# Kernel tuning notes

Measured on AMD Instinct MI355X. Metric: run time of the kernel, lower is better.

The kernel has to match this reference:

```python
import jax, jax.numpy as jnp
import numpy as np

N = 100000
D = 64
E = 1600000
EPS = 1e-5


def setup_inputs() -> dict:
    key = jax.random.key(0)
    k1, k2, k3, k4, k5, k6 = jax.random.split(key, 6)
    node_features = jax.random.normal(k1, (N, D), dtype=jnp.float32)
    edge_index = jax.random.randint(k2, (E, 2), 0, N, dtype=jnp.int64)
    # torch Linear params: W [out, in], b [out]
    lim_m = 1.0 / np.sqrt(2 * D)
    W_msg = jax.random.uniform(k3, (D, 2 * D), minval=-lim_m, maxval=lim_m, dtype=jnp.float32)
    b_msg = jax.random.uniform(k4, (D,), minval=-lim_m, maxval=lim_m, dtype=jnp.float32)
    W_upd = jax.random.uniform(k5, (D, 2 * D), minval=-lim_m, maxval=lim_m, dtype=jnp.float32)
    b_upd = jax.random.uniform(k6, (D,), minval=-lim_m, maxval=lim_m, dtype=jnp.float32)
    gamma = jnp.ones((D,), dtype=jnp.float32)
    beta = jnp.zeros((D,), dtype=jnp.float32)
    return {
        "node_features": node_features,
        "edge_index": edge_index,
        "W_msg": W_msg,
        "b_msg": b_msg,
        "W_upd": W_upd,
        "b_upd": b_upd,
        "gamma": gamma,
        "beta": beta,
    }


def _layer_norm(x, gamma, beta):
    mu = jnp.mean(x, axis=-1, keepdims=True)
    var = jnp.mean(jnp.square(x - mu), axis=-1, keepdims=True)
    return (x - mu) * jax.lax.rsqrt(var + EPS) * gamma + beta


def reference(node_features, edge_index, W_msg, b_msg, W_upd, b_upd, gamma, beta):
    src = edge_index[:, 0]
    tgt = edge_index[:, 1]
    # per-edge message: relu(Linear(cat(x[src], x[tgt])))  -- split weight to avoid [E,2D] concat
    Wm_s = W_msg[:, :D]  # [D, D] applied to src feats
    Wm_t = W_msg[:, D:]  # [D, D] applied to tgt feats
    msg = jax.nn.relu(node_features[src] @ Wm_s.T + node_features[tgt] @ Wm_t.T + b_msg)  # [E, D]
    # scatter-mean into target nodes
    messages = jax.ops.segment_sum(msg, tgt, num_segments=N)  # [N, D]
    counts = jax.ops.segment_sum(jnp.ones((edge_index.shape[0],), dtype=node_features.dtype), tgt, num_segments=N)
    counts = jnp.maximum(counts, 1.0)[:, None]
    messages = messages / counts
    # update: relu(Linear(cat(x, messages))) + residual + LayerNorm
    Wu_x = W_upd[:, :D]
    Wu_m = W_upd[:, D:]
    updated = jax.nn.relu(node_features @ Wu_x.T + messages @ Wu_m.T + b_upd)
    return _layer_norm(updated + node_features, gamma, beta)
```

## Files before the change

### kernel.cpp

```cpp
#include <hip/hip_runtime.h>
#include <hip/hip_bf16.h>
#include <stdint.h>

#define NNODES 100000
#define DF 64
#define NEDGES 1600000
#define ND (NNODES * DF)
#define BKT 100
#define NBUCK 1000
#define CHUNK 128
#define NCHUNK (NEDGES / CHUNK)

static __device__ __forceinline__ float bf2f(unsigned short u) {
    union { uint32_t i; float f; } c; c.i = ((uint32_t)u) << 16; return c.f;
}
static __device__ __forceinline__ void unpack2(uint32_t u, float& lo, float& hi) {
    union { uint32_t i; float f; } a, b;
    a.i = u << 16; b.i = u & 0xFFFF0000u;
    lo = a.f; hi = b.f;
}

__global__ void detect_k(const unsigned short* __restrict__ x,
                         const unsigned int* __restrict__ ei,
                         int* __restrict__ flags) {
    __shared__ int cnt_sane, cnt_odd_nz;
    if (threadIdx.x == 0) { cnt_sane = 0; cnt_odd_nz = 0; }
    __syncthreads();
    unsigned short s = x[threadIdx.x * 2];
    unsigned short m = s & 0x7FFF;
    if (m < 0x0080 || (m >= 0x3000 && m <= 0x4200)) atomicAdd(&cnt_sane, 1);
    if (threadIdx.x < 64) {
        if (ei[threadIdx.x * 2 + 1] != 0u) atomicAdd(&cnt_odd_nz, 1);
    }
    __syncthreads();
    if (threadIdx.x == 0) {
        flags[0] = (cnt_sane >= 192) ? 1 : 0;
        flags[1] = (cnt_odd_nz == 0) ? 1 : 0;
    }
}

__global__ void wconv_k(const int* __restrict__ flags,
                        const void* __restrict__ Wm, const void* __restrict__ Wu,
                        const void* __restrict__ bm, const void* __restrict__ bu,
                        const void* __restrict__ ga, const void* __restrict__ be,
                        float* __restrict__ WfM, float* __restrict__ WfU,
                        float* __restrict__ prm) {
    const int bf = flags[0];
    int i = blockIdx.x * 256 + threadIdx.x;
    if (i < 16384) {
        const void* src = (i < 8192) ? Wm : Wu;
        float* dst = (i < 8192) ? WfM : WfU;
        int ii = i & 8191, j = ii >> 6, k = ii & 63;
        int si = (j & 63) * 128 + ((j >> 6) ? 64 : 0) + k;
        dst[ii] = bf ? bf2f(((const unsigned short*)src)[si]) : ((const float*)src)[si];
    } else if (i < 16384 + 256) {
        int t = i - 16384, which = t >> 6, k = t & 63;
        const void* p = (which == 0) ? bm : (which == 1) ? bu : (which == 2) ? ga : be;
        prm[t] = bf ? bf2f(((const unsigned short*)p)[k]) : ((const float*)p)[k];
    }
}

__global__ __launch_bounds__(256) void proj_k(const int* __restrict__ flags,
                                              const void* __restrict__ xv,
                                              const float* __restrict__ WfM,
                                              const float* __restrict__ prm,
                                              __hip_bfloat16* __restrict__ Ps,
                                              __hip_bfloat16* __restrict__ Pt) {
    const int bf = flags[0];
    const int lane = threadIdx.x & 63;
    const int wib = __builtin_amdgcn_readfirstlane(threadIdx.x >> 6);

    float wsr[64], wtr[64];
    {
        const float* r0 = WfM + lane * 64;
        const float* r1 = WfM + (64 + lane) * 64;
        #pragma unroll
        for (int k = 0; k < 64; ++k) { wsr[k] = r0[k]; wtr[k] = r1[k]; }
    }
    const float bm = prm[lane];

    for (int n = blockIdx.x * 4 + wib; n < NNODES; n += gridDim.x * 4) {
        float as0 = 0.f, as1 = 0.f, at0 = 0.f, at1 = 0.f;
        if (bf) {
            const uint32_t* xw = (const uint32_t*)((const unsigned short*)xv + (size_t)n * DF);
            #pragma unroll
            for (int d = 0; d < 32; ++d) {
                float x0, x1; unpack2(xw[d], x0, x1);
                as0 = fmaf(x0, wsr[2*d],   as0);
                as1 = fmaf(x1, wsr[2*d+1], as1);
                at0 = fmaf(x0, wtr[2*d],   at0);
                at1 = fmaf(x1, wtr[2*d+1], at1);
            }
        } else {
            const float* xf = (const float*)xv + (size_t)n * DF;
            #pragma unroll
            for (int d = 0; d < 64; d += 2) {
                as0 = fmaf(xf[d],   wsr[d],   as0);
                as1 = fmaf(xf[d+1], wsr[d+1], as1);
                at0 = fmaf(xf[d],   wtr[d],   at0);
                at1 = fmaf(xf[d+1], wtr[d+1], at1);
            }
        }
        Ps[(size_t)n * DF + lane] = __float2bfloat16(as0 + as1);
        Pt[(size_t)n * DF + lane] = __float2bfloat16(at0 + at1 + bm);
    }
}

__global__ __launch_bounds__(256) void bhist_k(const int* __restrict__ flags,
                                               const int* __restrict__ ei,
                                               int* __restrict__ BktCnt) {
    __shared__ int h[NBUCK];
    const int i64 = flags[1];
    for (int i = threadIdx.x; i < NBUCK; i += 256) h[i] = 0;
    __syncthreads();
    int stride = gridDim.x * 256;
    for (int e = blockIdx.x * 256 + threadIdx.x; e < NEDGES; e += stride) {
        int tgt = i64 ? ei[4*e + 2] : ei[2*e + 1];
        if ((unsigned)tgt < NNODES) atomicAdd(&h[tgt / BKT], 1);
    }
    __syncthreads();
    for (int b = threadIdx.x; b < NBUCK; b += 256)
        if (h[b]) atomicAdd(BktCnt + b, h[b]);
}

__global__ __launch_bounds__(1024) void bscan_k(const int* __restrict__ BktCnt,
                                                int* __restrict__ BktOff,
                                                int* __restrict__ BktCur) {
    __shared__ int lds[1024];
    int t = threadIdx.x;
    int c = (t < NBUCK) ? BktCnt[t] : 0;
    lds[t] = c;
    __syncthreads();
    for (int off = 1; off < 1024; off <<= 1) {
        int add = (t >= off) ? lds[t - off] : 0;
        __syncthreads();
        lds[t] += add;
        __syncthreads();
    }
    if (t < NBUCK) {
        int ex = lds[t] - c;
        BktOff[t] = ex;
        BktCur[t] = ex;
    }
    if (t == NBUCK - 1) BktOff[NBUCK] = lds[t];
}

__global__ __launch_bounds__(256) void bfill_k(const int* __restrict__ flags,
                                               const int* __restrict__ ei,
                                               int* __restrict__ BktCur,
                                               int* __restrict__ BktE) {
    __shared__ int h[NBUCK], h2[NBUCK], basee[NBUCK];
    const int i64 = flags[1];
    for (int i = threadIdx.x; i < NBUCK; i += 256) { h[i] = 0; h2[i] = 0; }
    __syncthreads();
    const int stride = gridDim.x * 256;
    for (int e = blockIdx.x * 256 + threadIdx.x; e < NEDGES; e += stride) {
        int tgt = i64 ? ei[4*e + 2] : ei[2*e + 1];
        if ((unsigned)tgt < NNODES) atomicAdd(&h[tgt / BKT], 1);
    }
    __syncthreads();
    for (int b = threadIdx.x; b < NBUCK; b += 256)
        if (h[b]) basee[b] = atomicAdd(BktCur + b, h[b]);
    __syncthreads();
    for (int e = blockIdx.x * 256 + threadIdx.x; e < NEDGES; e += stride) {
        int src, tgt;
        if (i64) { src = ei[4*e]; tgt = ei[4*e + 2]; }
        else     { src = ei[2*e]; tgt = ei[2*e + 1]; }
        if ((unsigned)tgt >= NNODES) continue;
        int b = tgt / BKT;
        int tl = tgt - b * BKT;
        int r = atomicAdd(&h2[b], 1);
        BktE[basee[b] + r] = (tl << 24) | (src & 0xFFFFFF);
    }
}

__global__ __launch_bounds__(256) void tsort_k(const int* __restrict__ BktOff,
                                               const int* __restrict__ BktE,
                                               int* __restrict__ CsrSrc,
                                               int* __restrict__ Row) {
    __shared__ int oc[128], excl[128], cur[128];
    const int tid = threadIdx.x;
    const int b = blockIdx.x;
    const int s = BktOff[b], e = BktOff[b + 1];
    const int n = e - s;
    if (tid < 128) { oc[tid] = 0; }
    __syncthreads();
    for (int i = tid; i < n; i += 256)
        atomicAdd(&oc[((unsigned)BktE[s + i]) >> 24], 1);
    __syncthreads();
    if (tid < 128) excl[tid] = (tid > 0) ? oc[tid - 1] : 0;
    __syncthreads();
    for (int off = 1; off < 128; off <<= 1) {
        int add = (tid >= off && tid < 128) ? excl[tid - off] : 0;
        __syncthreads();
        if (tid < 128) excl[tid] += add;
        __syncthreads();
    }
    if (tid < BKT) {
        Row[b * BKT + tid] = s + excl[tid];
        cur[tid] = excl[tid];
    }
    if (b == 0 && tid == 0) Row[NNODES] = NEDGES;
    __syncthreads();
    for (int i = tid; i < n; i += 256) {
        int v = BktE[s + i];
        int tl = ((unsigned)v) >> 24;
        int p = atomicAdd(&cur[tl], 1);
        CsrSrc[s + p] = v & 0xFFFFFF;
    }
}

__global__ __launch_bounds__(256) void agg_k(const __hip_bfloat16* __restrict__ Ps,
                                             const __hip_bfloat16* __restrict__ Pt,
                                             const int* __restrict__ Row,
                                             const int* __restrict__ CsrSrc,
                                             __hip_bfloat16* __restrict__ Msg) {
    const int lane = threadIdx.x & 63;
    const int wib = __builtin_amdgcn_readfirstlane(threadIdx.x >> 6);
    const int w = blockIdx.x * 4 + wib;
    if (w >= NCHUNK) return;
    const int eA = w * CHUNK;
    const int hiB = (w == NCHUNK - 1) ? (NEDGES + 1) : (eA + CHUNK);

    int lo = 0, hi = NNODES + 1;
    while (lo < hi) { int mid = (lo + hi) >> 1; if (Row[mid] >= eA) hi = mid; else lo = mid + 1; }
    const int t_lo = lo;
    lo = t_lo; hi = NNODES + 1;
    while (lo < hi) { int mid = (lo + hi) >> 1; if (Row[mid] >= hiB) hi = mid; else lo = mid + 1; }
    int t_hi = lo;
    if (t_hi > NNODES) t_hi = NNODES;

    const unsigned short* Ps16 = (const unsigned short*)Ps;
    const unsigned short* Pt16 = (const unsigned short*)Pt;

    for (int t = t_lo; t < t_hi; ++t) {
        const int segS = Row[t], segE = Row[t + 1];
        const int deg = segE - segS;
        float pt = bf2f(Pt16[(size_t)t * DF + lane]);
        float macc = 0.f;
        int i = segS;
        for (; i + 8 <= segE; i += 8) {
            int s0 = CsrSrc[i+0], s1 = CsrSrc[i+1], s2 = CsrSrc[i+2], s3 = CsrSrc[i+3];
            int s4 = CsrSrc[i+4], s5 = CsrSrc[i+5], s6 = CsrSrc[i+6], s7 = CsrSrc[i+7];
            if ((unsigned)s0 >= NNODES) s0 = 0;
            if ((unsigned)s1 >= NNODES) s1 = 0;
            if ((unsigned)s2 >= NNODES) s2 = 0;
            if ((unsigned)s3 >= NNODES) s3 = 0;
            if ((unsigned)s4 >= NNODES) s4 = 0;
            if ((unsigned)s5 >= NNODES) s5 = 0;
            if ((unsigned)s6 >= NNODES) s6 = 0;
            if ((unsigned)s7 >= NNODES) s7 = 0;
            float p0 = bf2f(Ps16[(size_t)s0 * DF + lane]);
            float p1 = bf2f(Ps16[(size_t)s1 * DF + lane]);
            float p2 = bf2f(Ps16[(size_t)s2 * DF + lane]);
            float p3 = bf2f(Ps16[(size_t)s3 * DF + lane]);
            float p4 = bf2f(Ps16[(size_t)s4 * DF + lane]);
            float p5 = bf2f(Ps16[(size_t)s5 * DF + lane]);
            float p6 = bf2f(Ps16[(size_t)s6 * DF + lane]);
            float p7 = bf2f(Ps16[(size_t)s7 * DF + lane]);
            macc += fmaxf(p0 + pt, 0.f) + fmaxf(p1 + pt, 0.f)
                  + fmaxf(p2 + pt, 0.f) + fmaxf(p3 + pt, 0.f)
                  + fmaxf(p4 + pt, 0.f) + fmaxf(p5 + pt, 0.f)
                  + fmaxf(p6 + pt, 0.f) + fmaxf(p7 + pt, 0.f);
        }
        for (; i < segE; ++i) {
            int s0 = CsrSrc[i];
            if ((unsigned)s0 >= NNODES) s0 = 0;
            macc += fmaxf(bf2f(Ps16[(size_t)s0 * DF + lane]) + pt, 0.f);
        }
        float mval = (deg > 0) ? (macc / (float)deg) : 0.f;
        Msg[(size_t)t * DF + lane] = __float2bfloat16(mval);
    }
}

__global__ __launch_bounds__(256) void upd_k(const int* __restrict__ flags,
                                             const void* __restrict__ xv,
                                             const __hip_bfloat16* __restrict__ Msg,
                                             const float* __restrict__ WfU,
                                             const float* __restrict__ prm,
                                             void* __restrict__ outv) {
    const int bf = flags[0];
    const int lane = threadIdx.x & 63;
    const int wib = __builtin_amdgcn_readfirstlane(threadIdx.x >> 6);

    float wx[64], wm[64];
    {
        const float* r0 = WfU + lane * 64;
        const float* r1 = WfU + (lane + 64) * 64;
        #pragma unroll
        for (int k = 0; k < 64; ++k) { wx[k] = r0[k]; wm[k] = r1[k]; }
    }
    const float bu = prm[64 + lane];
    const float ga = prm[128 + lane];
    const float be = prm[192 + lane];

    for (int n = blockIdx.x * 4 + wib; n < NNODES; n += gridDim.x * 4) {
        float da0 = 0.f, da1 = 0.f, db0 = 0.f, db1 = 0.f;
        float xl;
        if (bf) {
            const uint32_t* xw = (const uint32_t*)((const unsigned short*)xv + (size_t)n * DF);
            #pragma unroll
            for (int d = 0; d < 32; ++d) {
                float x0, x1; unpack2(xw[d], x0, x1);
                da0 = fmaf(x0, wx[2*d],   da0);
                da1 = fmaf(x1, wx[2*d+1], da1);
            }
            xl = bf2f(((const unsigned short*)xv)[(size_t)n * DF + lane]);
        } else {
            const float* xf = (const float*)xv + (size_t)n * DF;
            #pragma unroll
            for (int d = 0; d < 64; d += 2) {
                da0 = fmaf(xf[d],   wx[d],   da0);
                da1 = fmaf(xf[d+1], wx[d+1], da1);
            }
            xl = ((const float*)xv)[(size_t)n * DF + lane];
        }
        {
            const uint32_t* mw = (const uint32_t*)((const unsigned short*)Msg + (size_t)n * DF);
            #pragma unroll
            for (int d = 0; d < 32; ++d) {
                float m0, m1; unpack2(mw[d], m0, m1);
                db0 = fmaf(m0, wm[2*d],   db0);
                db1 = fmaf(m1, wm[2*d+1], db1);
            }
        }
        float u = fmaxf((da0 + da1) + (db0 + db1) + bu, 0.f);
        float r = u + xl;

        float s = r, s2 = r * r;
        #pragma unroll
        for (int m = 1; m < 64; m <<= 1) {
            s  += __shfl_xor(s, m, 64);
            s2 += __shfl_xor(s2, m, 64);
        }
        float mu  = s * (1.0f / 64.0f);
        float var = fmaxf(s2 * (1.0f / 64.0f) - mu * mu, 0.f);
        float o = (r - mu) * rsqrtf(var + 1e-5f) * ga + be;

        size_t gi = (size_t)n * DF + lane;
        if (bf) ((__hip_bfloat16*)outv)[gi] = __float2bfloat16(o);
        else    ((float*)outv)[gi] = o;
    }
}

extern "C" void kernel_launch(void* const* d_in, const int* in_sizes, int n_in,
                              void* d_out, int out_size, void* d_ws, size_t ws_size,
                              hipStream_t stream) {
    const void* x  = d_in[0];
    const int*  ei = (const int*)d_in[1];
    const void* Wm = d_in[2];
    const void* bm = d_in[3];
    const void* Wu = d_in[4];
    const void* bu = d_in[5];
    const void* ga = d_in[6];
    const void* be = d_in[7];

    char* ws = (char*)d_ws;
    size_t off = 0;
    __hip_bfloat16* Ps  = (__hip_bfloat16*)(ws + off); off += (size_t)ND * 2;
    __hip_bfloat16* Pt  = (__hip_bfloat16*)(ws + off); off += (size_t)ND * 2;
    __hip_bfloat16* Msg = (__hip_bfloat16*)(ws + off); off += (size_t)ND * 2;
    int*   BktE   = (int*)(ws + off); off += (size_t)NEDGES * 4;
    int*   CsrSrc = (int*)(ws + off); off += (size_t)NEDGES * 4;
    int*   Row    = (int*)(ws + off); off += (size_t)(NNODES + 1) * 4;
    int*   BktCnt = (int*)(ws + off); off += NBUCK * 4;
    int*   BktOff = (int*)(ws + off); off += (NBUCK + 1) * 4;
    int*   BktCur = (int*)(ws + off); off += NBUCK * 4;
    int*   flg    = (int*)(ws + off); off += 16;
    float* WfM    = (float*)(ws + off); off += 8192 * 4;
    float* WfU    = (float*)(ws + off); off += 8192 * 4;
    float* prm    = (float*)(ws + off); off += 256 * 4;

    (void)hipMemsetAsync(BktCnt, 0, NBUCK * 4, stream);

    detect_k<<<1, 256, 0, stream>>>((const unsigned short*)x, (const unsigned int*)ei, flg);
    wconv_k<<<65, 256, 0, stream>>>(flg, Wm, Wu, bm, bu, ga, be, WfM, WfU, prm);

    proj_k<<<1563, 256, 0, stream>>>(flg, x, WfM, prm, Ps, Pt);

    bhist_k<<<256, 256, 0, stream>>>(flg, ei, BktCnt);
    bscan_k<<<1, 1024, 0, stream>>>(BktCnt, BktOff, BktCur);
    bfill_k<<<128, 256, 0, stream>>>(flg, ei, BktCur, BktE);
    tsort_k<<<NBUCK, 256, 0, stream>>>(BktOff, BktE, CsrSrc, Row);

    agg_k<<<(NCHUNK + 3) / 4, 256, 0, stream>>>(Ps, Pt, Row, CsrSrc, Msg);

    upd_k<<<1563, 256, 0, stream>>>(flg, x, Msg, WfU, prm, d_out);
}
```

Measured before the change: 375.2 us.

## Remap projection and update kernels to one node per thread with LDS weights

Both dense per-node kernels switch from one wavefront per node (a lane per output feature, weights held in registers, shuffle-reduced LayerNorm) to one thread per node. Each thread loads its 64-feature row with vector loads, reads weights broadcast from shared memory, and writes packed bf16 or float4 rows. LayerNorm is now computed inside the thread with no cross-lane shuffles. The block only has 391 blocks of 256 threads. Per-thread register arrays are large and each block needs 32KB of LDS, so occupancy and spills could hurt, and row-strided per-thread global accesses are uncoalesced across lanes.

```diff
diff --git a/kernel.cpp b/kernel.cpp
--- a/kernel.cpp
+++ b/kernel.cpp
@@ -18,6 +18,11 @@
     union { uint32_t i; float f; } a, b;
     a.i = u << 16; b.i = u & 0xFFFF0000u;
     lo = a.f; hi = b.f;
+}
+static __device__ __forceinline__ uint32_t pkbf2(float lo, float hi) {
+    union { __hip_bfloat16 b; unsigned short u; } a, b2;
+    a.b = __float2bfloat16(lo); b2.b = __float2bfloat16(hi);
+    return ((uint32_t)b2.u << 16) | (uint32_t)a.u;
 }
 
 __global__ void detect_k(const unsigned short* __restrict__ x,
@@ -60,49 +65,77 @@
     }
 }
 
-__global__ __launch_bounds__(256) void proj_k(const int* __restrict__ flags,
-                                              const void* __restrict__ xv,
-                                              const float* __restrict__ WfM,
-                                              const float* __restrict__ prm,
-                                              __hip_bfloat16* __restrict__ Ps,
-                                              __hip_bfloat16* __restrict__ Pt) {
+__global__ __launch_bounds__(256, 2) void proj_k(const int* __restrict__ flags,
+                                                 const void* __restrict__ xv,
+                                                 const float* __restrict__ WfM,
+                                                 const float* __restrict__ prm,
+                                                 __hip_bfloat16* __restrict__ Ps,
+                                                 __hip_bfloat16* __restrict__ Pt) {
+    __shared__ float wlds[8192];
+    __shared__ float blds[64];
+    for (int i = threadIdx.x; i < 8192; i += 256) wlds[i] = WfM[i];
+    if (threadIdx.x < 64) blds[threadIdx.x] = prm[threadIdx.x];
+    __syncthreads();
     const int bf = flags[0];
-    const int lane = threadIdx.x & 63;
-    const int wib = __builtin_amdgcn_readfirstlane(threadIdx.x >> 6);
-
-    float wsr[64], wtr[64];
-    {
-        const float* r0 = WfM + lane * 64;
-        const float* r1 = WfM + (64 + lane) * 64;
-        #pragma unroll
-        for (int k = 0; k < 64; ++k) { wsr[k] = r0[k]; wtr[k] = r1[k]; }
-    }
-    const float bm = prm[lane];
-
-    for (int n = blockIdx.x * 4 + wib; n < NNODES; n += gridDim.x * 4) {
-        float as0 = 0.f, as1 = 0.f, at0 = 0.f, at1 = 0.f;
-        if (bf) {
-            const uint32_t* xw = (const uint32_t*)((const unsigned short*)xv + (size_t)n * DF);
+    const int n = blockIdx.x * 256 + threadIdx.x;
+    if (n >= NNODES) return;
+
+    float xr[64];
+    if (bf) {
+        const uint4* xw = (const uint4*)((const unsigned short*)xv + (size_t)n * DF);
+        #pragma unroll
+        for (int q = 0; q < 8; ++q) {
+            uint4 v = xw[q];
+            unpack2(v.x, xr[8*q+0], xr[8*q+1]);
+            unpack2(v.y, xr[8*q+2], xr[8*q+3]);
+            unpack2(v.z, xr[8*q+4], xr[8*q+5]);
+            unpack2(v.w, xr[8*q+6], xr[8*q+7]);
+        }
+    } else {
+        const float4* xf = (const float4*)((const float*)xv + (size_t)n * DF);
+        #pragma unroll
+        for (int q = 0; q < 16; ++q) {
+            float4 v = xf[q];
+            xr[4*q+0] = v.x; xr[4*q+1] = v.y; xr[4*q+2] = v.z; xr[4*q+3] = v.w;
+        }
+    }
+
+    uint32_t pso[32], pto[32];
+    #pragma unroll
+    for (int jp = 0; jp < 32; ++jp) {
+        float sv0, sv1, tv0, tv1;
+        #pragma unroll
+        for (int h = 0; h < 2; ++h) {
+            const int j = 2*jp + h;
+            const float4* ws4 = (const float4*)(wlds + j * 64);
+            const float4* wt4 = (const float4*)(wlds + (64 + j) * 64);
+            float a0=0.f,a1=0.f,a2=0.f,a3=0.f,b0=0.f,b1=0.f,b2=0.f,b3=0.f;
             #pragma unroll
-            for (int d = 0; d < 32; ++d) {
-                float x0, x1; unpack2(xw[d], x0, x1);
-                as0 = fmaf(x0, wsr[2*d],   as0);
-                as1 = fmaf(x1, wsr[2*d+1], as1);
-                at0 = fmaf(x0, wtr[2*d],   at0);
-                at1 = fmaf(x1, wtr[2*d+1], at1);
+            for (int k = 0; k < 16; ++k) {
+                float4 w1 = ws4[k];
+                float4 w2 = wt4[k];
+                a0 = fmaf(xr[4*k+0], w1.x, a0);
+                a1 = fmaf(xr[4*k+1], w1.y, a1);
+                a2 = fmaf(xr[4*k+2], w1.z, a2);
+                a3 = fmaf(xr[4*k+3], w1.w, a3);
+                b0 = fmaf(xr[4*k+0], w2.x, b0);
+                b1 = fmaf(xr[4*k+1], w2.y, b1);
+                b2 = fmaf(xr[4*k+2], w2.z, b2);
+                b3 = fmaf(xr[4*k+3], w2.w, b3);
             }
-        } else {
-            const float* xf = (const float*)xv + (size_t)n * DF;
-            #pragma unroll
-            for (int d = 0; d < 64; d += 2) {
-                as0 = fmaf(xf[d],   wsr[d],   as0);
-                as1 = fmaf(xf[d+1], wsr[d+1], as1);
-                at0 = fmaf(xf[d],   wtr[d],   at0);
-                at1 = fmaf(xf[d+1], wtr[d+1], at1);
-            }
-        }
-        Ps[(size_t)n * DF + lane] = __float2bfloat16(as0 + as1);
-        Pt[(size_t)n * DF + lane] = __float2bfloat16(at0 + at1 + bm);
+            float sv = (a0+a1)+(a2+a3);
+            float tv = (b0+b1)+(b2+b3) + blds[j];
+            if (h == 0) { sv0 = sv; tv0 = tv; } else { sv1 = sv; tv1 = tv; }
+        }
+        pso[jp] = pkbf2(sv0, sv1);
+        pto[jp] = pkbf2(tv0, tv1);
+    }
+    uint4* po = (uint4*)((unsigned short*)Ps + (size_t)n * DF);
+    uint4* pt = (uint4*)((unsigned short*)Pt + (size_t)n * DF);
+    #pragma unroll
+    for (int q = 0; q < 8; ++q) {
+        po[q] = make_uint4(pso[4*q+0], pso[4*q+1], pso[4*q+2], pso[4*q+3]);
+        pt[q] = make_uint4(pto[4*q+0], pto[4*q+1], pto[4*q+2], pto[4*q+3]);
     }
 }
 
@@ -273,73 +306,106 @@
     }
 }
 
-__global__ __launch_bounds__(256) void upd_k(const int* __restrict__ flags,
-                                             const void* __restrict__ xv,
-                                             const __hip_bfloat16* __restrict__ Msg,
-                                             const float* __restrict__ WfU,
-                                             const float* __restrict__ prm,
-                                             void* __restrict__ outv) {
+__global__ __launch_bounds__(256, 2) void upd_k(const int* __restrict__ flags,
+                                                const void* __restrict__ xv,
+                                                const __hip_bfloat16* __restrict__ Msg,
+                                                const float* __restrict__ WfU,
+                                                const float* __restrict__ prm,
+                                                void* __restrict__ outv) {
+    __shared__ float wlds[8192];
+    __shared__ float plds[192];
+    for (int i = threadIdx.x; i < 8192; i += 256) wlds[i] = WfU[i];
+    if (threadIdx.x < 192) plds[threadIdx.x] = prm[64 + threadIdx.x];
+    __syncthreads();
     const int bf = flags[0];
-    const int lane = threadIdx.x & 63;
-    const int wib = __builtin_amdgcn_readfirstlane(threadIdx.x >> 6);
-
-    float wx[64], wm[64];
+    const int n = blockIdx.x * 256 + threadIdx.x;
+    if (n >= NNODES) return;
+
+    float xr[64], mr[64];
+    if (bf) {
+        const uint4* xw = (const uint4*)((const unsigned short*)xv + (size_t)n * DF);
+        #pragma unroll
+        for (int q = 0; q < 8; ++q) {
+            uint4 v = xw[q];
+            unpack2(v.x, xr[8*q+0], xr[8*q+1]);
+            unpack2(v.y, xr[8*q+2], xr[8*q+3]);
+            unpack2(v.z, xr[8*q+4], xr[8*q+5]);
+            unpack2(v.w, xr[8*q+6], xr[8*q+7]);
+        }
+    } else {
+        const float4* xf = (const float4*)((const float*)xv + (size_t)n * DF);
+        #pragma unroll
+        for (int q = 0; q < 16; ++q) {
+            float4 v = xf[q];
+            xr[4*q+0] = v.x; xr[4*q+1] = v.y; xr[4*q+2] = v.z; xr[4*q+3] = v.w;
+        }
+    }
     {
-        const float* r0 = WfU + lane * 64;
-        const float* r1 = WfU + (lane + 64) * 64;
-        #pragma unroll
-        for (int k = 0; k < 64; ++k) { wx[k] = r0[k]; wm[k] = r1[k]; }
-    }
-    const float bu = prm[64 + lane];
-    const float ga = prm[128 + lane];
-    const float be = prm[192 + lane];
-
-    for (int n = blockIdx.x * 4 + wib; n < NNODES; n += gridDim.x * 4) {
-        float da0 = 0.f, da1 = 0.f, db0 = 0.f, db1 = 0.f;
-        float xl;
-        if (bf) {
-            const uint32_t* xw = (const uint32_t*)((const unsigned short*)xv + (size_t)n * DF);
-            #pragma unroll
-            for (int d = 0; d < 32; ++d) {
-                float x0, x1; unpack2(xw[d], x0, x1);
-                da0 = fmaf(x0, wx[2*d],   da0);
-                da1 = fmaf(x1, wx[2*d+1], da1);
-            }
-            xl = bf2f(((const unsigned short*)xv)[(size_t)n * DF + lane]);
-        } else {
-            const float* xf = (const float*)xv + (size_t)n * DF;
-            #pragma unroll
-            for (int d = 0; d < 64; d += 2) {
-                da0 = fmaf(xf[d],   wx[d],   da0);
-                da1 = fmaf(xf[d+1], wx[d+1], da1);
-            }
-            xl = ((const float*)xv)[(size_t)n * DF + lane];
-        }
-        {
-            const uint32_t* mw = (const uint32_t*)((const unsigned short*)Msg + (size_t)n * DF);
-            #pragma unroll
-            for (int d = 0; d < 32; ++d) {
-                float m0, m1; unpack2(mw[d], m0, m1);
-                db0 = fmaf(m0, wm[2*d],   db0);
-                db1 = fmaf(m1, wm[2*d+1], db1);
-            }
-        }
-        float u = fmaxf((da0 + da1) + (db0 + db1) + bu, 0.f);
-        float r = u + xl;
-
-        float s = r, s2 = r * r;
-        #pragma unroll
-        for (int m = 1; m < 64; m <<= 1) {
-            s  += __shfl_xor(s, m, 64);
-            s2 += __shfl_xor(s2, m, 64);
-        }
-        float mu  = s * (1.0f / 64.0f);
-        float var = fmaxf(s2 * (1.0f / 64.0f) - mu * mu, 0.f);
-        float o = (r - mu) * rsqrtf(var + 1e-5f) * ga + be;
-
-        size_t gi = (size_t)n * DF + lane;
-        if (bf) ((__hip_bfloat16*)outv)[gi] = __float2bfloat16(o);
-        else    ((float*)outv)[gi] = o;
+        const uint4* mw = (const uint4*)((const unsigned short*)Msg + (size_t)n * DF);
+        #pragma unroll
+        for (int q = 0; q < 8; ++q) {
+            uint4 v = mw[q];
+            unpack2(v.x, mr[8*q+0], mr[8*q+1]);
+            unpack2(v.y, mr[8*q+2], mr[8*q+3]);
+            unpack2(v.z, mr[8*q+4], mr[8*q+5]);
+            unpack2(v.w, mr[8*q+6], mr[8*q+7]);
+        }
+    }
+
+    float rr[64];
+    float s = 0.f, s2 = 0.f;
+    #pragma unroll
+    for (int j = 0; j < 64; ++j) {
+        const float4* wx4 = (const float4*)(wlds + j * 64);
+        const float4* wm4 = (const float4*)(wlds + (64 + j) * 64);
+        float a0=0.f,a1=0.f,a2=0.f,a3=0.f,b0=0.f,b1=0.f,b2=0.f,b3=0.f;
+        #pragma unroll
+        for (int k = 0; k < 16; ++k) {
+            float4 w1 = wx4[k];
+            float4 w2 = wm4[k];
+            a0 = fmaf(xr[4*k+0], w1.x, a0);
+            a1 = fmaf(xr[4*k+1], w1.y, a1);
+            a2 = fmaf(xr[4*k+2], w1.z, a2);
+            a3 = fmaf(xr[4*k+3], w1.w, a3);
+            b0 = fmaf(mr[4*k+0], w2.x, b0);
+            b1 = fmaf(mr[4*k+1], w2.y, b1);
+            b2 = fmaf(mr[4*k+2], w2.z, b2);
+            b3 = fmaf(mr[4*k+3], w2.w, b3);
+        }
+        float u = fmaxf((a0+a1)+(a2+a3) + (b0+b1)+(b2+b3) + plds[j], 0.f);
+        float r = u + xr[j];
+        rr[j] = r;
+        s += r;
+        s2 = fmaf(r, r, s2);
+    }
+
+    float mu  = s  * (1.0f / 64.0f);
+    float var = fmaxf(s2 * (1.0f / 64.0f) - mu * mu, 0.f);
+    float kv  = rsqrtf(var + 1e-5f);
+
+    if (bf) {
+        uint32_t ob[32];
+        #pragma unroll
+        for (int jp = 0; jp < 32; ++jp) {
+            float o0 = (rr[2*jp+0] - mu) * kv * plds[64 + 2*jp+0] + plds[128 + 2*jp+0];
+            float o1 = (rr[2*jp+1] - mu) * kv * plds[64 + 2*jp+1] + plds[128 + 2*jp+1];
+            ob[jp] = pkbf2(o0, o1);
+        }
+        uint4* po = (uint4*)((unsigned short*)outv + (size_t)n * DF);
+        #pragma unroll
+        for (int q = 0; q < 8; ++q)
+            po[q] = make_uint4(ob[4*q+0], ob[4*q+1], ob[4*q+2], ob[4*q+3]);
+    } else {
+        float4* po = (float4*)((float*)outv + (size_t)n * DF);
+        #pragma unroll
+        for (int q = 0; q < 16; ++q) {
+            float4 v;
+            v.x = (rr[4*q+0] - mu) * kv * plds[64 + 4*q+0] + plds[128 + 4*q+0];
+            v.y = (rr[4*q+1] - mu) * kv * plds[64 + 4*q+1] + plds[128 + 4*q+1];
+            v.z = (rr[4*q+2] - mu) * kv * plds[64 + 4*q+2] + plds[128 + 4*q+2];
+            v.w = (rr[4*q+3] - mu) * kv * plds[64 + 4*q+3] + plds[128 + 4*q+3];
+            po[q] = v;
+        }
     }
 }
 
@@ -376,7 +442,7 @@
     detect_k<<<1, 256, 0, stream>>>((const unsigned short*)x, (const unsigned int*)ei, flg);
     wconv_k<<<65, 256, 0, stream>>>(flg, Wm, Wu, bm, bu, ga, be, WfM, WfU, prm);
 
-    proj_k<<<1563, 256, 0, stream>>>(flg, x, WfM, prm, Ps, Pt);
+    proj_k<<<(NNODES + 255) / 256, 256, 0, stream>>>(flg, x, WfM, prm, Ps, Pt);
 
     bhist_k<<<256, 256, 0, stream>>>(flg, ei, BktCnt);
     bscan_k<<<1, 1024, 0, stream>>>(BktCnt, BktOff, BktCur);
@@ -385,5 +451,5 @@
 
     agg_k<<<(NCHUNK + 3) / 4, 256, 0, stream>>>(Ps, Pt, Row, CsrSrc, Msg);
 
-    upd_k<<<1563, 256, 0, stream>>>(flg, x, Msg, WfU, prm, d_out);
-}
+    upd_k<<<(NNODES + 255) / 256, 256, 0, stream>>>(flg, x, Msg, WfU, prm, d_out);
+}
```

Result: faster. 365.8 us (-2.5%).

## Split fused node matmuls into single-weight kernels with transposed weights and vector loads

Applied to the files above, without the earlier changes.

The dual-projection kernel, which held two 64-float weight rows per lane, is replaced by a generic single-matrix kernel launched once for Ps and once for Pt. Each launch keeps only 64 weight registers, and the weights are loaded through a transposed layout so lanes read them coalesced. The update step is split the same way: x@Wu_x + bias goes into a float temporary that reuses the Ps/Pt workspace, and a second kernel adds the Msg projection, residual and LayerNorm. Node rows are now read with 128-bit vector loads. The aim is lower register pressure and cheaper loads, at the cost of reading x more than once and writing and re-reading a full fp32 intermediate.

```diff
diff --git a/kernel.cpp b/kernel.cpp
--- a/kernel.cpp
+++ b/kernel.cpp
@@ -43,66 +43,72 @@
                         const void* __restrict__ Wm, const void* __restrict__ Wu,
                         const void* __restrict__ bm, const void* __restrict__ bu,
                         const void* __restrict__ ga, const void* __restrict__ be,
-                        float* __restrict__ WfM, float* __restrict__ WfU,
+                        float* __restrict__ WfMT, float* __restrict__ WfUT,
                         float* __restrict__ prm) {
     const int bf = flags[0];
     int i = blockIdx.x * 256 + threadIdx.x;
     if (i < 16384) {
         const void* src = (i < 8192) ? Wm : Wu;
-        float* dst = (i < 8192) ? WfM : WfU;
+        float* dst = (i < 8192) ? WfMT : WfUT;
         int ii = i & 8191, j = ii >> 6, k = ii & 63;
         int si = (j & 63) * 128 + ((j >> 6) ? 64 : 0) + k;
-        dst[ii] = bf ? bf2f(((const unsigned short*)src)[si]) : ((const float*)src)[si];
-    } else if (i < 16384 + 256) {
+        float v = bf ? bf2f(((const unsigned short*)src)[si]) : ((const float*)src)[si];
+        dst[(j >> 6) * 4096 + k * 64 + (j & 63)] = v;
+    } else if (i < 16384 + 320) {
         int t = i - 16384, which = t >> 6, k = t & 63;
-        const void* p = (which == 0) ? bm : (which == 1) ? bu : (which == 2) ? ga : be;
-        prm[t] = bf ? bf2f(((const unsigned short*)p)[k]) : ((const float*)p)[k];
-    }
-}
-
-__global__ __launch_bounds__(256) void proj_k(const int* __restrict__ flags,
-                                              const void* __restrict__ xv,
-                                              const float* __restrict__ WfM,
-                                              const float* __restrict__ prm,
-                                              __hip_bfloat16* __restrict__ Ps,
-                                              __hip_bfloat16* __restrict__ Pt) {
-    const int bf = flags[0];
+        if (which == 4) { prm[t] = 0.f; }
+        else {
+            const void* p = (which == 0) ? bm : (which == 1) ? bu : (which == 2) ? ga : be;
+            prm[t] = bf ? bf2f(((const unsigned short*)p)[k]) : ((const float*)p)[k];
+        }
+    }
+}
+
+__global__ __launch_bounds__(256, 1) void mm_k(const int* __restrict__ flags,
+                                               const void* __restrict__ xv,
+                                               const float* __restrict__ WT,
+                                               const float* __restrict__ bias,
+                                               void* __restrict__ outv,
+                                               int of) {
     const int lane = threadIdx.x & 63;
     const int wib = __builtin_amdgcn_readfirstlane(threadIdx.x >> 6);
-
-    float wsr[64], wtr[64];
-    {
-        const float* r0 = WfM + lane * 64;
-        const float* r1 = WfM + (64 + lane) * 64;
-        #pragma unroll
-        for (int k = 0; k < 64; ++k) { wsr[k] = r0[k]; wtr[k] = r1[k]; }
-    }
-    const float bm = prm[lane];
-
-    for (int n = blockIdx.x * 4 + wib; n < NNODES; n += gridDim.x * 4) {
-        float as0 = 0.f, as1 = 0.f, at0 = 0.f, at1 = 0.f;
+    const int bf = flags[0];
+
+    float w[64];
+    #pragma unroll
+    for (int k = 0; k < 64; ++k) w[k] = WT[k * 64 + lane];
+    const float bs = bias[lane];
+
+    const int wv = blockIdx.x * 4 + wib;
+    const int nw = gridDim.x * 4;
+    for (int n = wv; n < NNODES; n += nw) {
+        float a0 = 0.f, a1 = 0.f, a2 = 0.f, a3 = 0.f;
         if (bf) {
-            const uint32_t* xw = (const uint32_t*)((const unsigned short*)xv + (size_t)n * DF);
+            const uint4* xr = (const uint4*)((const unsigned short*)xv + (size_t)n * DF);
             #pragma unroll
-            for (int d = 0; d < 32; ++d) {
-                float x0, x1; unpack2(xw[d], x0, x1);
-                as0 = fmaf(x0, wsr[2*d],   as0);
-                as1 = fmaf(x1, wsr[2*d+1], as1);
-                at0 = fmaf(x0, wtr[2*d],   at0);
-                at1 = fmaf(x1, wtr[2*d+1], at1);
+            for (int q = 0; q < 8; ++q) {
+                uint4 v = xr[q];
+                float x0,x1,x2,x3,x4,x5,x6,x7;
+                unpack2(v.x, x0, x1); unpack2(v.y, x2, x3);
+                unpack2(v.z, x4, x5); unpack2(v.w, x6, x7);
+                a0 = fmaf(x0, w[8*q+0], a0); a1 = fmaf(x1, w[8*q+1], a1);
+                a2 = fmaf(x2, w[8*q+2], a2); a3 = fmaf(x3, w[8*q+3], a3);
+                a0 = fmaf(x4, w[8*q+4], a0); a1 = fmaf(x5, w[8*q+5], a1);
+                a2 = fmaf(x6, w[8*q+6], a2); a3 = fmaf(x7, w[8*q+7], a3);
             }
         } else {
-            const float* xf = (const float*)xv + (size_t)n * DF;
+            const float4* xr = (const float4*)((const float*)xv + (size_t)n * DF);
             #pragma unroll
-            for (int d = 0; d < 64; d += 2) {
-                as0 = fmaf(xf[d],   wsr[d],   as0);
-                as1 = fmaf(xf[d+1], wsr[d+1], as1);
-                at0 = fmaf(xf[d],   wtr[d],   at0);
-                at1 = fmaf(xf[d+1], wtr[d+1], at1);
+            for (int q = 0; q < 16; ++q) {
+                float4 v = xr[q];
+                a0 = fmaf(v.x, w[4*q+0], a0); a1 = fmaf(v.y, w[4*q+1], a1);
+                a2 = fmaf(v.z, w[4*q+2], a2); a3 = fmaf(v.w, w[4*q+3], a3);
             }
         }
-        Ps[(size_t)n * DF + lane] = __float2bfloat16(as0 + as1);
-        Pt[(size_t)n * DF + lane] = __float2bfloat16(at0 + at1 + bm);
+        float r = (a0 + a1) + (a2 + a3) + bs;
+        size_t gi = (size_t)n * DF + lane;
+        if (of) ((float*)outv)[gi] = r;
+        else    ((__hip_bfloat16*)outv)[gi] = __float2bfloat16(r);
     }
 }
 
@@ -273,58 +279,46 @@
     }
 }
 
-__global__ __launch_bounds__(256) void upd_k(const int* __restrict__ flags,
-                                             const void* __restrict__ xv,
-                                             const __hip_bfloat16* __restrict__ Msg,
-                                             const float* __restrict__ WfU,
-                                             const float* __restrict__ prm,
-                                             void* __restrict__ outv) {
-    const int bf = flags[0];
+__global__ __launch_bounds__(256, 1) void u2_k(const int* __restrict__ flags,
+                                               const void* __restrict__ xv,
+                                               const __hip_bfloat16* __restrict__ Msg,
+                                               const float* __restrict__ t1,
+                                               const float* __restrict__ WT,
+                                               const float* __restrict__ prm,
+                                               void* __restrict__ outv) {
     const int lane = threadIdx.x & 63;
     const int wib = __builtin_amdgcn_readfirstlane(threadIdx.x >> 6);
-
-    float wx[64], wm[64];
-    {
-        const float* r0 = WfU + lane * 64;
-        const float* r1 = WfU + (lane + 64) * 64;
-        #pragma unroll
-        for (int k = 0; k < 64; ++k) { wx[k] = r0[k]; wm[k] = r1[k]; }
-    }
-    const float bu = prm[64 + lane];
+    const int bf = flags[0];
+
+    float w[64];
+    #pragma unroll
+    for (int k = 0; k < 64; ++k) w[k] = WT[k * 64 + lane];
     const float ga = prm[128 + lane];
     const float be = prm[192 + lane];
 
-    for (int n = blockIdx.x * 4 + wib; n < NNODES; n += gridDim.x * 4) {
-        float da0 = 0.f, da1 = 0.f, db0 = 0.f, db1 = 0.f;
-        float xl;
-        if (bf) {
-            const uint32_t* xw = (const uint32_t*)((const unsigned short*)xv + (size_t)n * DF);
-            #pragma unroll
-            for (int d = 0; d < 32; ++d) {
-                float x0, x1; unpack2(xw[d], x0, x1);
-                da0 = fmaf(x0, wx[2*d],   da0);
-                da1 = fmaf(x1, wx[2*d+1], da1);
-            }
-            xl = bf2f(((const unsigned short*)xv)[(size_t)n * DF + lane]);
-        } else {
-            const float* xf = (const float*)xv + (size_t)n * DF;
-            #pragma unroll
-            for (int d = 0; d < 64; d += 2) {
-                da0 = fmaf(xf[d],   wx[d],   da0);
-                da1 = fmaf(xf[d+1], wx[d+1], da1);
-            }
-            xl = ((const float*)xv)[(size_t)n * DF + lane];
-        }
-        {
-            const uint32_t* mw = (const uint32_t*)((const unsigned short*)Msg + (size_t)n * DF);
-            #pragma unroll
-            for (int d = 0; d < 32; ++d) {
-                float m0, m1; unpack2(mw[d], m0, m1);
-                db0 = fmaf(m0, wm[2*d],   db0);
-                db1 = fmaf(m1, wm[2*d+1], db1);
-            }
-        }
-        float u = fmaxf((da0 + da1) + (db0 + db1) + bu, 0.f);
+    const unsigned short* x16 = (const unsigned short*)xv;
+    const float* xf = (const float*)xv;
+
+    const int wv = blockIdx.x * 4 + wib;
+    const int nw = gridDim.x * 4;
+    for (int n = wv; n < NNODES; n += nw) {
+        float b0 = 0.f, b1 = 0.f, b2 = 0.f, b3 = 0.f;
+        const uint4* mw = (const uint4*)((const unsigned short*)Msg + (size_t)n * DF);
+        #pragma unroll
+        for (int q = 0; q < 8; ++q) {
+            uint4 v = mw[q];
+            float m0,m1,m2,m3,m4,m5,m6,m7;
+            unpack2(v.x, m0, m1); unpack2(v.y, m2, m3);
+            unpack2(v.z, m4, m5); unpack2(v.w, m6, m7);
+            b0 = fmaf(m0, w[8*q+0], b0); b1 = fmaf(m1, w[8*q+1], b1);
+            b2 = fmaf(m2, w[8*q+2], b2); b3 = fmaf(m3, w[8*q+3], b3);
+            b0 = fmaf(m4, w[8*q+4], b0); b1 = fmaf(m5, w[8*q+5], b1);
+            b2 = fmaf(m6, w[8*q+6], b2); b3 = fmaf(m7, w[8*q+7], b3);
+        }
+        size_t gi = (size_t)n * DF + lane;
+        float t  = t1[gi];
+        float xl = bf ? bf2f(x16[gi]) : xf[gi];
+        float u = fmaxf((b0 + b1) + (b2 + b3) + t, 0.f);
         float r = u + xl;
 
         float s = r, s2 = r * r;
@@ -337,7 +331,6 @@
         float var = fmaxf(s2 * (1.0f / 64.0f) - mu * mu, 0.f);
         float o = (r - mu) * rsqrtf(var + 1e-5f) * ga + be;
 
-        size_t gi = (size_t)n * DF + lane;
         if (bf) ((__hip_bfloat16*)outv)[gi] = __float2bfloat16(o);
         else    ((float*)outv)[gi] = o;
     }
@@ -367,16 +360,19 @@
     int*   BktOff = (int*)(ws + off); off += (NBUCK + 1) * 4;
     int*   BktCur = (int*)(ws + off); off += NBUCK * 4;
     int*   flg    = (int*)(ws + off); off += 16;
-    float* WfM    = (float*)(ws + off); off += 8192 * 4;
-    float* WfU    = (float*)(ws + off); off += 8192 * 4;
-    float* prm    = (float*)(ws + off); off += 256 * 4;
+    float* WfMT   = (float*)(ws + off); off += 8192 * 4;
+    float* WfUT   = (float*)(ws + off); off += 8192 * 4;
+    float* prm    = (float*)(ws + off); off += 320 * 4;
+
+    float* t1 = (float*)Ps;
 
     (void)hipMemsetAsync(BktCnt, 0, NBUCK * 4, stream);
 
     detect_k<<<1, 256, 0, stream>>>((const unsigned short*)x, (const unsigned int*)ei, flg);
-    wconv_k<<<65, 256, 0, stream>>>(flg, Wm, Wu, bm, bu, ga, be, WfM, WfU, prm);
-
-    proj_k<<<1563, 256, 0, stream>>>(flg, x, WfM, prm, Ps, Pt);
+    wconv_k<<<65, 256, 0, stream>>>(flg, Wm, Wu, bm, bu, ga, be, WfMT, WfUT, prm);
+
+    mm_k<<<1024, 256, 0, stream>>>(flg, x, WfMT,        prm + 256, Ps, 0);
+    mm_k<<<1024, 256, 0, stream>>>(flg, x, WfMT + 4096, prm,       Pt, 0);
 
     bhist_k<<<256, 256, 0, stream>>>(flg, ei, BktCnt);
     bscan_k<<<1, 1024, 0, stream>>>(BktCnt, BktOff, BktCur);
@@ -385,5 +381,7 @@
 
     agg_k<<<(NCHUNK + 3) / 4, 256, 0, stream>>>(Ps, Pt, Row, CsrSrc, Msg);
 
-    upd_k<<<1563, 256, 0, stream>>>(flg, x, Msg, WfU, prm, d_out);
-}
+    mm_k<<<1024, 256, 0, stream>>>(flg, x, WfUT, prm + 64, t1, 1);
+
+    u2_k<<<1024, 256, 0, stream>>>(flg, x, Msg, t1, WfUT + 4096, prm, d_out);
+}
```

After: 338.8 us. 9.7% less time.
